# Performance work log

Measured on AMD Instinct MI355X. Metric: run time of the kernel, lower is better.

The kernel has to match this reference:

```python
import jax, jax.numpy as jnp
import numpy as np

Q = 2.0
TEMPERATURE = 1.0
EXP = 1.0 / (Q - 1.0)  # exponent 1/(q-1); q=2 -> sparsemax-style projection
N_BISECT_ITERS = 50    # enough for xtol ~ 1e-6 over an interval of width ~ (u_max - u_min + 10)


def setup_inputs() -> dict:
    key = jax.random.key(0)
    k_x, k_w1, k_w2 = jax.random.split(key, 3)
    B, D, H, E = 8192, 4096, 256, 64
    x = jax.random.normal(k_x, (B, D), dtype=jnp.float32)
    w1 = jax.random.normal(k_w1, (D, H), dtype=jnp.float32) * 0.02
    b1 = jnp.zeros((H,), dtype=jnp.float32)
    w2 = jax.random.normal(k_w2, (H, E), dtype=jnp.float32) * 0.05
    b2 = jnp.zeros((E,), dtype=jnp.float32)
    return {"x": x, "w1": w1, "b1": b1, "w2": w2, "b2": b2}


def _bisect_tau(us):
    # us: [B, E] = utilities / temperature. Find per-row tau with sum(relu(us - tau)**EXP) = 1.
    lo = jnp.min(us, axis=-1) - 10.0   # constraint(lo) > 0
    hi = jnp.max(us, axis=-1)          # constraint(hi) = -1 < 0

    def body(i, carry):
        lo, hi = carry
        mid = 0.5 * (lo + hi)
        f = jnp.sum(jnp.maximum(us - mid[..., None], 0.0) ** EXP, axis=-1) - 1.0
        pos = f > 0.0  # constraint is decreasing in tau: root is above mid
        return (jnp.where(pos, mid, lo), jnp.where(pos, hi, mid))

    lo, hi = jax.lax.fori_loop(0, N_BISECT_ITERS, body, (lo, hi))
    return 0.5 * (lo + hi)  # [B]


def reference(x, w1, b1, w2, b2):
    # utility_net (Dropout is identity in eval mode)
    h = jax.nn.relu(x @ w1 + b1)            # [B, 256]
    utilities = h @ w2 + b2                  # [B, E]
    us = utilities / TEMPERATURE
    # tau is found by root-finding on detached values in the original (.item()),
    # so it is a constant w.r.t. differentiation.
    tau = jax.lax.stop_gradient(_bisect_tau(jax.lax.stop_gradient(us)))
    p = jnp.maximum(us - tau[..., None], 0.0) ** EXP   # [B, E]
    p = p / (jnp.sum(p, axis=-1, keepdims=True) + 1e-8)
    return p
```

## Files before the change

### kernel.cpp

```cpp
#include <hip/hip_runtime.h>
#include <stdint.h>

typedef _Float16 f16;
typedef _Float16 f16x8 __attribute__((ext_vector_type(8)));
typedef _Float16 f16x4 __attribute__((ext_vector_type(4)));
typedef float f32x4 __attribute__((ext_vector_type(4)));

#define D_DIM 4096
#define H_DIM 256
#define E_DIM 64
#define BM 32
#define BK 64
#define NKT 64

__global__ void pack_kernel(const float* __restrict__ w1, f16* __restrict__ w1s,
                            const float* __restrict__ w2, f16* __restrict__ w2s) {
  const int b = blockIdx.x;
  const int t = threadIdx.x;
  if (b < 512) {
    const int u = b * 256 + t;
    const int lane = u & 63;
    const int kk = (u >> 6) & 1;
    const int c16 = (u >> 7) & 15;
    const int kt = u >> 11;
    const int g = lane >> 4, r = lane & 15;
    const int k0 = kt * 64 + kk * 32 + g * 8;
    const int col = c16 * 16 + r;
    f16x8 o;
#pragma unroll
    for (int j = 0; j < 8; ++j) o[j] = (f16)w1[(size_t)(k0 + j) * H_DIM + col];
    *(f16x8*)(w1s + (size_t)u * 8) = o;
  } else {
    const int u = (b - 512) * 256 + t;
    const int lane = u & 63;
    const int ks = (u >> 6) & 7;
    const int cg = u >> 9;
    const int g = lane >> 4, r = lane & 15;
    const int k0 = ks * 32 + g * 8;
    const int col = cg * 16 + r;
    f16x8 o;
#pragma unroll
    for (int j = 0; j < 8; ++j) o[j] = (f16)w2[(size_t)(k0 + j) * E_DIM + col];
    *(f16x8*)(w2s + (size_t)u * 8) = o;
  }
}

__launch_bounds__(512)
__global__ void fused_kernel(const float* __restrict__ x,
                             const f16* __restrict__ w1s,
                             const float* __restrict__ b1,
                             const f16* __restrict__ w2s,
                             const float* __restrict__ b2,
                             float* __restrict__ out) {
  __shared__ __align__(16) char smem[24576];
  f16* As = (f16*)smem;
  f16* h_lds = (f16*)smem;
  float* u_lds = (float*)(smem + 16384);

  const int t = threadIdx.x;
  const int lane = t & 63;
  const int wn = t >> 6;
  const int g = lane >> 4, r = lane & 15;
  const int brow = blockIdx.x * BM;

  const int a_row = t >> 4;
  const int a_col = (t & 15) << 2;
  const int a_sw = a_col ^ ((a_row & 7) << 3);
  const float* xrow = x + (size_t)(brow + a_row) * D_DIM + a_col;
  const f16* bptr = w1s + (size_t)(wn * 2) * 1024 + lane * 8;

  f32x4 acc[2][2] = {{{0.f,0.f,0.f,0.f},{0.f,0.f,0.f,0.f}},
                     {{0.f,0.f,0.f,0.f},{0.f,0.f,0.f,0.f}}};
  f16x8 BA[8], BB[8];
  float4 xA[2], xB[2];

#define LDX(kt) (*(const float4*)(xrow + (size_t)(kt) * 64))
#define LDB(kt, B)                                                  \
  {                                                                 \
    const f16* p_ = bptr + (size_t)(kt) * 16384;                    \
    (B)[0] = *(const f16x8*)(p_);                                   \
    (B)[1] = *(const f16x8*)(p_ + 512);                             \
    (B)[2] = *(const f16x8*)(p_ + 1024);                            \
    (B)[3] = *(const f16x8*)(p_ + 1536);                            \
  }
#define STW(dst, v)                                                 \
  {                                                                 \
    f16x4 hv_;                                                      \
    hv_[0] = (f16)(v).x; hv_[1] = (f16)(v).y;                       \
    hv_[2] = (f16)(v).z; hv_[3] = (f16)(v).w;                       \
    *(f16x4*)((dst) + a_row * 64 + a_sw) = hv_;                     \
  }
#define COMP(Ab, B)                                                            \
  {                                                                            \
    _Pragma("unroll") for (int kk = 0; kk < 2; ++kk) {                         \
      const int kb_ = kk * 32 + g * 8;                                         \
      _Pragma("unroll") for (int rh = 0; rh < 2; ++rh) {                       \
        const int arow_ = rh * 16 + r;                                         \
        const f16x8 af_ =                                                      \
            *(const f16x8*)((Ab) + arow_ * 64 + (kb_ ^ ((arow_ & 7) << 3)));   \
        _Pragma("unroll") for (int ch = 0; ch < 2; ++ch) {                     \
          acc[rh][ch] = __builtin_amdgcn_mfma_f32_16x16x32_f16(                \
              af_, (B)[kk + ch * 2], acc[rh][ch], 0, 0, 0);                    \
        }                                                                      \
      }                                                                        \
    }                                                                          \
  }
#define BAR()                                          \
  asm volatile("s_waitcnt lgkmcnt(0)" ::: "memory");   \
  __builtin_amdgcn_s_barrier();

#define PHASE(s0, Bc, Bn, xc)                                     \
  {                                                               \
    STW(As + (((s0) + 2) & 3) * 2048, (xc)[0]);                   \
    STW(As + (((s0) + 3) & 3) * 2048, (xc)[1]);                   \
    {                                                             \
      int sx0 = (s0) + 6; if (sx0 > 63) sx0 = 63;                 \
      int sx1 = (s0) + 7; if (sx1 > 63) sx1 = 63;                 \
      (xc)[0] = LDX(sx0); (xc)[1] = LDX(sx1);                     \
    }                                                             \
    {                                                             \
      int sb0 = (s0) + 2; if (sb0 > 63) sb0 = 63;                 \
      int sb1 = (s0) + 3; if (sb1 > 63) sb1 = 63;                 \
      LDB(sb0, Bn); LDB(sb1, (Bn) + 4);                           \
    }                                                             \
    COMP(As + ((s0) & 3) * 2048, Bc);                             \
    COMP(As + (((s0) + 1) & 3) * 2048, (Bc) + 4);                 \
    BAR();                                                        \
  }

  {
    float4 t0 = LDX(0);
    float4 t1 = LDX(1);
    LDB(0, BA); LDB(1, BA + 4);
    xA[0] = LDX(2); xA[1] = LDX(3);
    xB[0] = LDX(4); xB[1] = LDX(5);
    STW(As, t0);
    STW(As + 2048, t1);
    BAR();
  }

#pragma unroll 1
  for (int pp = 0; pp < 16; ++pp) {
    const int s0 = pp * 4;
    PHASE(s0, BA, BB, xA);
    PHASE(s0 + 2, BB, BA, xB);
  }

#pragma unroll
  for (int rh = 0; rh < 2; ++rh)
#pragma unroll
    for (int ch = 0; ch < 2; ++ch) {
      const int col = wn * 32 + ch * 16 + r;
      const float bias = b1[col];
#pragma unroll
      for (int j = 0; j < 4; ++j) {
        const int row = rh * 16 + g * 4 + j;
        float v = acc[rh][ch][j] + bias;
        v = fmaxf(v, 0.f);
        h_lds[row * 256 + (col ^ ((row & 7) << 3))] = (f16)v;
      }
    }
  __syncthreads();

  const int rh2 = wn & 1;
  const int cg = wn >> 1;
  f32x4 acc2 = {0.f, 0.f, 0.f, 0.f};
  const f16* w2p = w2s + (size_t)(cg * 8) * 512 + lane * 8;
#pragma unroll
  for (int ks = 0; ks < 8; ++ks) {
    const int arow = rh2 * 16 + r;
    const int kb = ks * 32 + g * 8;
    const f16x8 af = *(const f16x8*)(h_lds + arow * 256 + (kb ^ ((arow & 7) << 3)));
    const f16x8 bf = *(const f16x8*)(w2p + ks * 512);
    acc2 = __builtin_amdgcn_mfma_f32_16x16x32_f16(af, bf, acc2, 0, 0, 0);
  }
  {
    const int col = cg * 16 + r;
    const float bias = b2[col];
#pragma unroll
    for (int j = 0; j < 4; ++j) {
      const int row = rh2 * 16 + g * 4 + j;
      u_lds[row * 64 + col] = acc2[j] + bias;
    }
  }
  __syncthreads();

  const int srow = wn * 4 + (lane >> 4);
  const int scol = (lane & 15) << 2;
  const float4 uv = *(const float4*)(u_lds + srow * 64 + scol);
  float u0 = uv.x, u1 = uv.y, u2 = uv.z, u3 = uv.w;

  float mx = fmaxf(fmaxf(u0, u1), fmaxf(u2, u3));
  float mn = fminf(fminf(u0, u1), fminf(u2, u3));
#pragma unroll
  for (int m = 1; m < 16; m <<= 1) {
    mx = fmaxf(mx, __shfl_xor(mx, m));
    mn = fminf(mn, __shfl_xor(mn, m));
  }
  float lo = mn - 10.0f, hi = mx;
#pragma unroll 1
  for (int it = 0; it < 32; ++it) {
    const float mid = 0.5f * (lo + hi);
    float s = fmaxf(u0 - mid, 0.f) + fmaxf(u1 - mid, 0.f) +
              fmaxf(u2 - mid, 0.f) + fmaxf(u3 - mid, 0.f);
#pragma unroll
    for (int m = 1; m < 16; m <<= 1) s += __shfl_xor(s, m);
    const bool pos = (s - 1.0f) > 0.0f;
    lo = pos ? mid : lo;
    hi = pos ? hi : mid;
  }
  const float tau = 0.5f * (lo + hi);
  const float p0 = fmaxf(u0 - tau, 0.f);
  const float p1 = fmaxf(u1 - tau, 0.f);
  const float p2 = fmaxf(u2 - tau, 0.f);
  const float p3 = fmaxf(u3 - tau, 0.f);
  float sum = p0 + p1 + p2 + p3;
#pragma unroll
  for (int m = 1; m < 16; m <<= 1) sum += __shfl_xor(sum, m);
  const float inv = 1.0f / (sum + 1e-8f);
  float4 pv;
  pv.x = p0 * inv; pv.y = p1 * inv; pv.z = p2 * inv; pv.w = p3 * inv;
  *(float4*)(out + (size_t)(brow + srow) * E_DIM + scol) = pv;
}

extern "C" void kernel_launch(void* const* d_in, const int* in_sizes, int n_in,
                              void* d_out, int out_size, void* d_ws, size_t ws_size,
                              hipStream_t stream) {
  const float* x  = (const float*)d_in[0];
  const float* w1 = (const float*)d_in[1];
  const float* b1 = (const float*)d_in[2];
  const float* w2 = (const float*)d_in[3];
  const float* b2 = (const float*)d_in[4];
  float* out = (float*)d_out;

  char* wsb = (char*)d_ws;
  f16* w1s = (f16*)wsb;
  f16* w2s = (f16*)(wsb + (2u << 20));

  pack_kernel<<<520, 256, 0, stream>>>(w1, w1s, w2, w2s);
  fused_kernel<<<8192 / BM, 512, 0, stream>>>(x, w1s, b1, w2s, b2, out);
}
```

Before: 54.44 us.

## Restructure GEMM1 mainloop with large x stages and 2x4 wave tiling

Rewrites the first GEMM's main loop. Each block now stages 512-wide K chunks of x into a double-buffered 64KB LDS region, giving 8 barriers in place of 32-ish. The 8 waves are rearranged into a 2x4 grid so each wave computes 16 rows by 64 columns, and B fragments are software-pipelined one K tile ahead. Launch bounds now request 2 blocks per CU. The aim is fewer barriers and deeper global-load latency hiding, at the cost of more registers and LDS, which may limit occupancy.

```diff
diff --git a/kernel.cpp b/kernel.cpp
--- a/kernel.cpp
+++ b/kernel.cpp
@@ -9,9 +9,6 @@
 #define D_DIM 4096
 #define H_DIM 256
 #define E_DIM 64
-#define BM 32
-#define BK 64
-#define NKT 64
 
 __global__ void pack_kernel(const float* __restrict__ w1, f16* __restrict__ w1s,
                             const float* __restrict__ w2, f16* __restrict__ w2s) {
@@ -45,121 +42,110 @@
   }
 }
 
-__launch_bounds__(512)
+__launch_bounds__(512, 2)
 __global__ void fused_kernel(const float* __restrict__ x,
                              const f16* __restrict__ w1s,
                              const float* __restrict__ b1,
                              const f16* __restrict__ w2s,
                              const float* __restrict__ b2,
                              float* __restrict__ out) {
-  __shared__ __align__(16) char smem[24576];
-  f16* As = (f16*)smem;
-  f16* h_lds = (f16*)smem;
-  float* u_lds = (float*)(smem + 16384);
+  __shared__ __align__(16) char smem[65536];
 
   const int t = threadIdx.x;
   const int lane = t & 63;
   const int wn = t >> 6;
+  const int wm = wn >> 2;
+  const int wc = wn & 3;
   const int g = lane >> 4, r = lane & 15;
-  const int brow = blockIdx.x * BM;
-
-  const int a_row = t >> 4;
-  const int a_col = (t & 15) << 2;
-  const int a_sw = a_col ^ ((a_row & 7) << 3);
-  const float* xrow = x + (size_t)(brow + a_row) * D_DIM + a_col;
-  const f16* bptr = w1s + (size_t)(wn * 2) * 1024 + lane * 8;
-
-  f32x4 acc[2][2] = {{{0.f,0.f,0.f,0.f},{0.f,0.f,0.f,0.f}},
-                     {{0.f,0.f,0.f,0.f},{0.f,0.f,0.f,0.f}}};
-  f16x8 BA[8], BB[8];
-  float4 xA[2], xB[2];
-
-#define LDX(kt) (*(const float4*)(xrow + (size_t)(kt) * 64))
-#define LDB(kt, B)                                                  \
-  {                                                                 \
-    const f16* p_ = bptr + (size_t)(kt) * 16384;                    \
-    (B)[0] = *(const f16x8*)(p_);                                   \
-    (B)[1] = *(const f16x8*)(p_ + 512);                             \
-    (B)[2] = *(const f16x8*)(p_ + 1024);                            \
-    (B)[3] = *(const f16x8*)(p_ + 1536);                            \
-  }
-#define STW(dst, v)                                                 \
-  {                                                                 \
-    f16x4 hv_;                                                      \
-    hv_[0] = (f16)(v).x; hv_[1] = (f16)(v).y;                       \
-    hv_[2] = (f16)(v).z; hv_[3] = (f16)(v).w;                       \
-    *(f16x4*)((dst) + a_row * 64 + a_sw) = hv_;                     \
-  }
-#define COMP(Ab, B)                                                            \
-  {                                                                            \
-    _Pragma("unroll") for (int kk = 0; kk < 2; ++kk) {                         \
-      const int kb_ = kk * 32 + g * 8;                                         \
-      _Pragma("unroll") for (int rh = 0; rh < 2; ++rh) {                       \
-        const int arow_ = rh * 16 + r;                                         \
-        const f16x8 af_ =                                                      \
-            *(const f16x8*)((Ab) + arow_ * 64 + (kb_ ^ ((arow_ & 7) << 3)));   \
-        _Pragma("unroll") for (int ch = 0; ch < 2; ++ch) {                     \
-          acc[rh][ch] = __builtin_amdgcn_mfma_f32_16x16x32_f16(                \
-              af_, (B)[kk + ch * 2], acc[rh][ch], 0, 0, 0);                    \
-        }                                                                      \
-      }                                                                        \
-    }                                                                          \
+  const int brow = blockIdx.x * 32;
+
+  const float* xt = x + (size_t)(brow + wn * 4) * D_DIM + lane * 4;
+  const f16* bptr = w1s + (size_t)(wc * 8) * 512 + lane * 8;
+
+  f32x4 acc[4] = {{0.f,0.f,0.f,0.f},{0.f,0.f,0.f,0.f},{0.f,0.f,0.f,0.f},{0.f,0.f,0.f,0.f}};
+  f16x8 Ba[8], Bb[8];
+  float4 xr[8];
+
+#define LDXS(s)                                                          \
+  {                                                                      \
+    _Pragma("unroll") for (int i = 0; i < 8; ++i)                        \
+      xr[i] = *(const float4*)(xt + (size_t)(i >> 1) * D_DIM +           \
+                               (s) * 512 + (i & 1) * 256);               \
+  }
+#define STW(dst)                                                         \
+  {                                                                      \
+    _Pragma("unroll") for (int i = 0; i < 8; ++i) {                      \
+      const int row_ = wn * 4 + (i >> 1);                                \
+      const int col_ = (i & 1) * 256 + lane * 4;                         \
+      f16x4 hv_;                                                         \
+      hv_[0] = (f16)xr[i].x; hv_[1] = (f16)xr[i].y;                      \
+      hv_[2] = (f16)xr[i].z; hv_[3] = (f16)xr[i].w;                      \
+      *(f16x4*)((dst) + row_ * 512 + (col_ ^ ((row_ & 7) << 3))) = hv_;  \
+    }                                                                    \
+  }
+#define LDB(kt, B)                                                       \
+  {                                                                      \
+    const f16* p_ = bptr + (size_t)(kt) * 16384;                         \
+    _Pragma("unroll") for (int q = 0; q < 8; ++q)                        \
+      (B)[q] = *(const f16x8*)(p_ + q * 512);                            \
+  }
+#define COMP_KT(bufp, j, B)                                              \
+  {                                                                      \
+    _Pragma("unroll") for (int kk = 0; kk < 2; ++kk) {                   \
+      const int row_ = wm * 16 + r;                                      \
+      const int kb_ = (j) * 64 + kk * 32 + g * 8;                        \
+      const f16x8 af_ =                                                  \
+          *(const f16x8*)((bufp) + row_ * 512 + (kb_ ^ ((row_ & 7) << 3))); \
+      _Pragma("unroll") for (int nf = 0; nf < 4; ++nf)                   \
+        acc[nf] = __builtin_amdgcn_mfma_f32_16x16x32_f16(                \
+            af_, (B)[nf * 2 + kk], acc[nf], 0, 0, 0);                    \
+    }                                                                    \
   }
 #define BAR()                                          \
   asm volatile("s_waitcnt lgkmcnt(0)" ::: "memory");   \
   __builtin_amdgcn_s_barrier();
-
-#define PHASE(s0, Bc, Bn, xc)                                     \
-  {                                                               \
-    STW(As + (((s0) + 2) & 3) * 2048, (xc)[0]);                   \
-    STW(As + (((s0) + 3) & 3) * 2048, (xc)[1]);                   \
-    {                                                             \
-      int sx0 = (s0) + 6; if (sx0 > 63) sx0 = 63;                 \
-      int sx1 = (s0) + 7; if (sx1 > 63) sx1 = 63;                 \
-      (xc)[0] = LDX(sx0); (xc)[1] = LDX(sx1);                     \
-    }                                                             \
-    {                                                             \
-      int sb0 = (s0) + 2; if (sb0 > 63) sb0 = 63;                 \
-      int sb1 = (s0) + 3; if (sb1 > 63) sb1 = 63;                 \
-      LDB(sb0, Bn); LDB(sb1, (Bn) + 4);                           \
-    }                                                             \
-    COMP(As + ((s0) & 3) * 2048, Bc);                             \
-    COMP(As + (((s0) + 1) & 3) * 2048, (Bc) + 4);                 \
-    BAR();                                                        \
-  }
-
-  {
-    float4 t0 = LDX(0);
-    float4 t1 = LDX(1);
-    LDB(0, BA); LDB(1, BA + 4);
-    xA[0] = LDX(2); xA[1] = LDX(3);
-    xB[0] = LDX(4); xB[1] = LDX(5);
-    STW(As, t0);
-    STW(As + 2048, t1);
+#define MIN63(v) ((v) > 63 ? 63 : (v))
+
+  LDXS(0);
+  LDB(0, Ba);
+  LDB(1, Bb);
+  STW((f16*)smem);
+  BAR();
+
+#pragma unroll 1
+  for (int s = 0; s < 8; ++s) {
+    f16* bc = (f16*)(smem + ((s & 1) << 15));
+    if (s < 7) LDXS(s + 1);
+    const int kt0 = s * 8;
+    COMP_KT(bc, 0, Ba); LDB(MIN63(kt0 + 2), Ba);
+    COMP_KT(bc, 1, Bb); LDB(MIN63(kt0 + 3), Bb);
+    COMP_KT(bc, 2, Ba); LDB(MIN63(kt0 + 4), Ba);
+    COMP_KT(bc, 3, Bb); LDB(MIN63(kt0 + 5), Bb);
+    COMP_KT(bc, 4, Ba); LDB(MIN63(kt0 + 6), Ba);
+    COMP_KT(bc, 5, Bb); LDB(MIN63(kt0 + 7), Bb);
+    COMP_KT(bc, 6, Ba); LDB(MIN63(kt0 + 8), Ba);
+    COMP_KT(bc, 7, Bb); LDB(MIN63(kt0 + 9), Bb);
     BAR();
-  }
-
-#pragma unroll 1
-  for (int pp = 0; pp < 16; ++pp) {
-    const int s0 = pp * 4;
-    PHASE(s0, BA, BB, xA);
-    PHASE(s0 + 2, BB, BA, xB);
-  }
-
-#pragma unroll
-  for (int rh = 0; rh < 2; ++rh)
-#pragma unroll
-    for (int ch = 0; ch < 2; ++ch) {
-      const int col = wn * 32 + ch * 16 + r;
-      const float bias = b1[col];
-#pragma unroll
-      for (int j = 0; j < 4; ++j) {
-        const int row = rh * 16 + g * 4 + j;
-        float v = acc[rh][ch][j] + bias;
-        v = fmaxf(v, 0.f);
-        h_lds[row * 256 + (col ^ ((row & 7) << 3))] = (f16)v;
-      }
+    if (s < 7) {
+      f16* bn = (f16*)(smem + (((s + 1) & 1) << 15));
+      STW(bn);
+      BAR();
     }
+  }
+
+  f16* h_lds = (f16*)smem;
+  float* u_lds = (float*)(smem + 16384);
+#pragma unroll
+  for (int nf = 0; nf < 4; ++nf) {
+    const int col = wc * 64 + nf * 16 + r;
+    const float bias = b1[col];
+#pragma unroll
+    for (int jj = 0; jj < 4; ++jj) {
+      const int row = wm * 16 + g * 4 + jj;
+      const float v = fmaxf(acc[nf][jj] + bias, 0.f);
+      h_lds[row * 256 + (col ^ ((row & 7) << 3))] = (f16)v;
+    }
+  }
   __syncthreads();
 
   const int rh2 = wn & 1;
@@ -167,11 +153,11 @@
   f32x4 acc2 = {0.f, 0.f, 0.f, 0.f};
   const f16* w2p = w2s + (size_t)(cg * 8) * 512 + lane * 8;
 #pragma unroll
-  for (int ks = 0; ks < 8; ++ks) {
+  for (int ksi = 0; ksi < 8; ++ksi) {
     const int arow = rh2 * 16 + r;
-    const int kb = ks * 32 + g * 8;
+    const int kb = ksi * 32 + g * 8;
     const f16x8 af = *(const f16x8*)(h_lds + arow * 256 + (kb ^ ((arow & 7) << 3)));
-    const f16x8 bf = *(const f16x8*)(w2p + ks * 512);
+    const f16x8 bf = *(const f16x8*)(w2p + ksi * 512);
     acc2 = __builtin_amdgcn_mfma_f32_16x16x32_f16(af, bf, acc2, 0, 0, 0);
   }
   {
@@ -179,8 +165,8 @@
     const float bias = b2[col];
 #pragma unroll
     for (int j = 0; j < 4; ++j) {
-      const int row = rh2 * 16 + g * 4 + j;
-      u_lds[row * 64 + col] = acc2[j] + bias;
+      const int rr = rh2 * 16 + g * 4 + j;
+      u_lds[rr * 64 + col] = acc2[j] + bias;
     }
   }
   __syncthreads();
@@ -201,11 +187,11 @@
 #pragma unroll 1
   for (int it = 0; it < 32; ++it) {
     const float mid = 0.5f * (lo + hi);
-    float s = fmaxf(u0 - mid, 0.f) + fmaxf(u1 - mid, 0.f) +
-              fmaxf(u2 - mid, 0.f) + fmaxf(u3 - mid, 0.f);
-#pragma unroll
-    for (int m = 1; m < 16; m <<= 1) s += __shfl_xor(s, m);
-    const bool pos = (s - 1.0f) > 0.0f;
+    float sm = fmaxf(u0 - mid, 0.f) + fmaxf(u1 - mid, 0.f) +
+               fmaxf(u2 - mid, 0.f) + fmaxf(u3 - mid, 0.f);
+#pragma unroll
+    for (int m = 1; m < 16; m <<= 1) sm += __shfl_xor(sm, m);
+    const bool pos = (sm - 1.0f) > 0.0f;
     lo = pos ? mid : lo;
     hi = pos ? hi : mid;
   }
@@ -238,5 +224,5 @@
   f16* w2s = (f16*)(wsb + (2u << 20));
 
   pack_kernel<<<520, 256, 0, stream>>>(w1, w1s, w2, w2s);
-  fused_kernel<<<8192 / BM, 512, 0, stream>>>(x, w1s, b1, w2s, b2, out);
+  fused_kernel<<<256, 512, 0, stream>>>(x, w1s, b1, w2s, b2, out);
 }
```

Measured after the change: 73.28 us. +34.6%, slower.
